# Kernel optimization log

Measured on AMD Instinct MI355X. Metric: run time of the kernel, lower is better.

The kernel has to match this reference:

```python
import jax, jax.numpy as jnp
import numpy as np

M, N, D, P, N_kv = 512, 4096, 128, 3584, 1024
H, H_kv = N // D, N_kv // D          # 32 query heads, 8 kv heads
G = H // H_kv                        # group size 4
L = P + M                            # cache length 4096


def setup_inputs() -> dict:
    key = jax.random.key(0)
    ks = jax.random.split(key, 6)
    w_scale = 0.008  # ~0.5/sqrt(N): keeps unscaled exp-softmax logits in fp32 range
    return {
        "X": jax.random.normal(ks[0], (M, N), jnp.float32),
        "W_q": jax.random.normal(ks[1], (N, N), jnp.float32) * w_scale,
        "W_k": jax.random.normal(ks[2], (N, N_kv), jnp.float32) * w_scale,
        "W_v": jax.random.normal(ks[3], (N, N_kv), jnp.float32) * w_scale,
        "cache_K": jax.random.normal(ks[4], (H, L, D), jnp.float32) * 0.02,
        "cache_V": jax.random.normal(ks[5], (H, L, D), jnp.float32) * 0.02,
    }


def reference(X, W_q, W_k, W_v, cache_K, cache_V):
    # fused QKV projection
    W_qkv = jnp.concatenate([W_q, W_k, W_v], axis=1)        # [N, N + 2*N_kv]
    qkv = X @ W_qkv                                          # [M, N + 2*N_kv]
    q = qkv[:, :N].reshape(M, H, D).transpose(1, 0, 2)       # [H, M, D]
    k = qkv[:, N:N + N_kv].reshape(M, H_kv, D).transpose(1, 0, 2)   # [H_kv, M, D]
    v = qkv[:, N + N_kv:].reshape(M, H_kv, D).transpose(1, 0, 2)    # [H_kv, M, D]
    # expand grouped KV heads (repeat_interleave) and append to cache at P
    k_exp = jnp.repeat(k, G, axis=0)                         # [H, M, D]
    v_exp = jnp.repeat(v, G, axis=0)
    Kc = cache_K.at[:, P:P + M, :].set(k_exp)                # [H, L, D]
    Vc = cache_V.at[:, P:P + M, :].set(v_exp)
    # naive (unscaled, non-max-subtracted) softmax attention over full cache
    scores = jnp.einsum('hmd,hld->hml', q, Kc)               # [H, M, L]
    e = jnp.exp(scores)
    weights = e / jnp.sum(e, axis=-1, keepdims=True)
    out = jnp.einsum('hml,hld->hmd', weights, Vc)            # [H, M, D]
    return out.transpose(1, 0, 2).reshape(M, H * D)          # [M, N]
```

## Files before the change

kernel.cpp:

```cpp
#include <hip/hip_runtime.h>

typedef __attribute__((ext_vector_type(8))) short short8;
typedef __attribute__((ext_vector_type(4))) float f32x4;

#define M_   512
#define N_   4096
#define D_   128
#define P_   3584
#define NKV  1024
#define L_   4096
#define H_   32

__device__ __forceinline__ ushort f2bf(float f) {
  union { float f; unsigned u; } v; v.f = f;
  unsigned r = (v.u + 0x7fffu + ((v.u >> 16) & 1u)) >> 16;
  return (ushort)r;
}
__device__ __forceinline__ float bf2f(ushort u) {
  union { unsigned u; float f; } v; v.u = ((unsigned)u) << 16;
  return v.f;
}

__device__ __forceinline__ void gload_lds16(const void* g, void* l) {
  __builtin_amdgcn_global_load_lds(
      (const __attribute__((address_space(1))) void*)g,
      (__attribute__((address_space(3))) void*)l, 16, 0, 0);
}

__global__ __launch_bounds__(256) void xconv(const float* __restrict__ X,
                                             ushort* __restrict__ Xs)
{
  int g = blockIdx.x * 256 + threadIdx.x;
  int row = g >> 9;
  int cir = g & 511;
  int grp = cir >> 3, ch = cir & 7;
  const float* src = &X[(size_t)row * 4096 + cir * 8];
  float4 f0 = *reinterpret_cast<const float4*>(src);
  float4 f1 = *reinterpret_cast<const float4*>(src + 4);
  short8 s;
  s[0] = f2bf(f0.x); s[1] = f2bf(f0.y); s[2] = f2bf(f0.z); s[3] = f2bf(f0.w);
  s[4] = f2bf(f1.x); s[5] = f2bf(f1.y); s[6] = f2bf(f1.z); s[7] = f2bf(f1.w);
  int dcol = grp * 64 + ((ch ^ (row & 7)) * 8);
  *reinterpret_cast<short8*>(&Xs[(size_t)row * 4096 + dcol]) = s;
}

__global__ __launch_bounds__(256) void wtrans(
    const float* __restrict__ Wq, const float* __restrict__ Wk,
    const float* __restrict__ Wv, ushort* __restrict__ Wt)
{
  int bx = blockIdx.x;
  int by = blockIdx.y;
  const float* W; int wcols, c0;
  if (by < 64)      { W = Wq; wcols = 4096; c0 = by * 64; }
  else if (by < 80) { W = Wk; wcols = 1024; c0 = (by - 64) * 64; }
  else              { W = Wv; wcols = 1024; c0 = (by - 80) * 64; }
  int orow0 = by * 64;
  int r0 = bx * 64;
  __shared__ float T[64][65];
  int tid = threadIdx.x;

  #pragma unroll
  for (int i = 0; i < 4; ++i) {
    int r = i * 16 + (tid >> 4);
    int c4 = tid & 15;
    float4 f = *reinterpret_cast<const float4*>(&W[(size_t)(r0 + r) * wcols + c0 + c4 * 4]);
    T[r][c4 * 4 + 0] = f.x; T[r][c4 * 4 + 1] = f.y;
    T[r][c4 * 4 + 2] = f.z; T[r][c4 * 4 + 3] = f.w;
  }
  __syncthreads();

  #pragma unroll
  for (int i = 0; i < 2; ++i) {
    int j = i * 256 + tid;
    int orr = j >> 3;
    int ch = j & 7;
    short8 s;
    #pragma unroll
    for (int e = 0; e < 8; ++e) s[e] = f2bf(T[ch * 8 + e][orr]);
    int orow = orow0 + orr;
    int dstch = ch ^ (orow & 7);
    *reinterpret_cast<short8*>(&Wt[(size_t)orow * 4096 + r0 + dstch * 8]) = s;
  }
}

#define GEMM_STAGE(buf, k0g) do {                                             \
    _Pragma("unroll")                                                         \
    for (int i_ = 0; i_ < 4; ++i_) {                                          \
      int blk_ = w * 4 + i_;                                                  \
      gload_lds16(Asrc + (size_t)(blk_ * 8 + (lane >> 3)) * 4096 + (k0g) + (lane & 7) * 8, \
                  &As[buf][blk_ * 512]);                                      \
    }                                                                         \
    _Pragma("unroll")                                                         \
    for (int i_ = 0; i_ < 4; ++i_) {                                          \
      int blk_ = w * 4 + i_;                                                  \
      gload_lds16(Bsrc + (size_t)(blk_ * 8 + (lane >> 3)) * 4096 + (k0g) + (lane & 7) * 8, \
                  &Bs[buf][blk_ * 512]);                                      \
    }                                                                         \
  } while (0)

__global__ __launch_bounds__(256, 2) void qkv_gemm3(
    const ushort* __restrict__ Xs, const ushort* __restrict__ Wt,
    float* __restrict__ pg)
{
  const int bx = blockIdx.x;
  const int by = blockIdx.y;
  const int bz = blockIdx.z;
  const int tid = threadIdx.x, lane = tid & 63, w = tid >> 6;
  const int wr = w >> 1, wc = w & 1;
  const int m0 = by * 128, n0 = bx * 128;
  const int kb0 = bz * 2048;

  __shared__ ushort As[2][128 * 64];
  __shared__ ushort Bs[2][128 * 64];

  f32x4 acc[4][4];
  #pragma unroll
  for (int m = 0; m < 4; ++m)
    #pragma unroll
    for (int n = 0; n < 4; ++n)
      acc[m][n] = (f32x4){0.f, 0.f, 0.f, 0.f};

  const ushort* Asrc = Xs + (size_t)m0 * 4096;
  const ushort* Bsrc = Wt + (size_t)n0 * 4096;

  GEMM_STAGE(0, kb0);
  __syncthreads();
  int cur = 0;

  for (int kt = 0; kt < 32; ++kt) {
    if (kt + 1 < 32) GEMM_STAGE(cur ^ 1, kb0 + (kt + 1) * 64);
    #pragma unroll
    for (int kk = 0; kk < 2; ++kk) {
      short8 a[4], b[4];
      #pragma unroll
      for (int m = 0; m < 4; ++m) {
        int row = wr * 64 + m * 16 + (lane & 15);
        int ch = (kk * 4 + (lane >> 4)) ^ (row & 7);
        a[m] = *reinterpret_cast<const short8*>(&As[cur][row * 64 + ch * 8]);
      }
      #pragma unroll
      for (int n = 0; n < 4; ++n) {
        int row = wc * 64 + n * 16 + (lane & 15);
        int ch = (kk * 4 + (lane >> 4)) ^ (row & 7);
        b[n] = *reinterpret_cast<const short8*>(&Bs[cur][row * 64 + ch * 8]);
      }
      #pragma unroll
      for (int m = 0; m < 4; ++m)
        #pragma unroll
        for (int n = 0; n < 4; ++n)
          acc[m][n] = __builtin_amdgcn_mfma_f32_16x16x32_bf16(a[m], b[n], acc[m][n], 0, 0, 0);
    }
    __syncthreads();
    cur ^= 1;
  }

  float* dst = pg + (size_t)bz * 512 * 6144;
  #pragma unroll
  for (int m = 0; m < 4; ++m)
    #pragma unroll
    for (int n = 0; n < 4; ++n)
      #pragma unroll
      for (int j = 0; j < 4; ++j) {
        int row = m0 + wr * 64 + m * 16 + (lane >> 4) * 4 + j;
        int col = n0 + wc * 64 + n * 16 + (lane & 15);
        dst[(size_t)row * 6144 + col] = acc[m][n][j];
      }
}

__global__ __launch_bounds__(256) void combine_qk(
    const float* __restrict__ pg, ushort* __restrict__ qb,
    ushort* __restrict__ Kb)
{
  int id = blockIdx.x * 256 + threadIdx.x;
  int m = id / 640;
  int c8 = (id - m * 640) * 8;
  const float* p0 = pg + (size_t)m * 6144 + c8;
  const float* p1 = p0 + (size_t)512 * 6144;
  short8 s;
  #pragma unroll
  for (int e = 0; e < 8; ++e) s[e] = f2bf(p0[e] + p1[e]);
  if (c8 < 4096) {
    *reinterpret_cast<short8*>(&qb[(size_t)m * 4096 + c8]) = s;
  } else {
    int o = c8 - 4096;
    int hk = o >> 7, d0 = o & 127;
    int l = P_ + m;
    int ch = (d0 >> 3) ^ (l & 7);
    #pragma unroll
    for (int g = 0; g < 4; ++g)
      *reinterpret_cast<short8*>(&Kb[((size_t)(hk * 4 + g) * L_ + l) * 128 + ch * 8]) = s;
  }
}

__global__ __launch_bounds__(256) void combine_v(
    const float* __restrict__ pg, ushort* __restrict__ Vtb)
{
  int bz = blockIdx.x;
  int mt = bz & 7, hk = (bz >> 3) & 7, dh = bz >> 6;
  int m0 = mt * 64, d0 = dh * 64;
  int colbase = 5120 + hk * 128 + d0;
  __shared__ float T[64][65];
  int tid = threadIdx.x;
  int r = tid >> 2, q4 = tid & 3;

  #pragma unroll
  for (int i = 0; i < 4; ++i) {
    int c = (q4 * 4 + i) * 4;
    const float* p0 = pg + (size_t)(m0 + r) * 6144 + colbase + c;
    const float* p1 = p0 + (size_t)512 * 6144;
    float4 a = *reinterpret_cast<const float4*>(p0);
    float4 b = *reinterpret_cast<const float4*>(p1);
    T[r][c + 0] = a.x + b.x; T[r][c + 1] = a.y + b.y;
    T[r][c + 2] = a.z + b.z; T[r][c + 3] = a.w + b.w;
  }
  __syncthreads();

  #pragma unroll
  for (int p = 0; p < 2; ++p) {
    int idx = p * 256 + tid;
    int dloc = idx >> 3, cc = idx & 7;
    short8 s;
    #pragma unroll
    for (int e = 0; e < 8; ++e) s[e] = f2bf(T[cc * 8 + e][dloc]);
    int d = d0 + dloc;
    int pc = (cc & 4) | ((cc ^ (d >> 1)) & 3);
    int l0 = P_ + m0;
    #pragma unroll
    for (int g = 0; g < 4; ++g) {
      int h = hk * 4 + g;
      *reinterpret_cast<short8*>(&Vtb[((size_t)h * 128 + d) * (size_t)L_ + l0 + pc * 8]) = s;
    }
  }
}

__global__ __launch_bounds__(256) void kconv(
    const float* __restrict__ cacheK, ushort* __restrict__ Kb)
{
  int h = blockIdx.x, lt = blockIdx.y;
  int tid = threadIdx.x;
  int r = tid >> 4, c = tid & 15;
  int l = lt * 16 + r;
  const float* src = &cacheK[((size_t)h * L_ + l) * 128 + c * 8];
  float4 f0 = *reinterpret_cast<const float4*>(src);
  float4 f1 = *reinterpret_cast<const float4*>(src + 4);
  short8 s;
  s[0] = f2bf(f0.x); s[1] = f2bf(f0.y); s[2] = f2bf(f0.z); s[3] = f2bf(f0.w);
  s[4] = f2bf(f1.x); s[5] = f2bf(f1.y); s[6] = f2bf(f1.z); s[7] = f2bf(f1.w);
  int pc = c ^ (l & 7);
  *reinterpret_cast<short8*>(&Kb[((size_t)h * L_ + l) * 128 + pc * 8]) = s;
}

__global__ __launch_bounds__(256) void vconv(
    const float* __restrict__ cacheV, ushort* __restrict__ Vtb)
{
  int h = blockIdx.x, lt = blockIdx.y, dh = blockIdx.z;
  int l0 = lt * 64, d0 = dh * 64;
  __shared__ float T[64][65];
  int tid = threadIdx.x;
  int r4 = tid >> 4, c = tid & 15;

  #pragma unroll
  for (int p = 0; p < 4; ++p) {
    int r = p * 16 + r4;
    float4 f = *reinterpret_cast<const float4*>(
        &cacheV[((size_t)h * L_ + l0 + r) * 128 + d0 + c * 4]);
    T[r][c * 4 + 0] = f.x; T[r][c * 4 + 1] = f.y;
    T[r][c * 4 + 2] = f.z; T[r][c * 4 + 3] = f.w;
  }
  __syncthreads();

  int dr = tid >> 2, part = tid & 3;
  int d = d0 + dr;
  #pragma unroll
  for (int q = 0; q < 2; ++q) {
    int cc = part * 2 + q;
    short8 s;
    #pragma unroll
    for (int e = 0; e < 8; ++e) s[e] = f2bf(T[cc * 8 + e][dr]);
    int pc = (cc & 4) | ((cc ^ (d >> 1)) & 3);
    *reinterpret_cast<short8*>(&Vtb[((size_t)h * 128 + d) * (size_t)L_ + l0 + pc * 8]) = s;
  }
}

#define ATTN_STAGE(buf, l0g) do {                                             \
    _Pragma("unroll")                                                         \
    for (int it_ = 0; it_ < 2; ++it_)                                         \
      gload_lds16(&Kb[kbase + (size_t)((l0g) + w * 8 + it_ * 4 + (lane >> 4)) * 128 + (lane & 15) * 8], \
                  &Ks[buf][(w * 8 + it_ * 4) * 128]);                         \
    _Pragma("unroll")                                                         \
    for (int it_ = 0; it_ < 2; ++it_)                                         \
      gload_lds16(&Vtb[vbase + (size_t)(w * 32 + it_ * 16 + (lane >> 2)) * (size_t)L_ + (l0g) + (lane & 3) * 8], \
                  &Vt[buf][(w * 32 + it_ * 16) * 32]);                        \
  } while (0)

#define ATTN_TILE(bufc) do {                                                  \
    f32x4 sc[2][2];                                                           \
    _Pragma("unroll")                                                         \
    for (int mb = 0; mb < 2; ++mb)                                            \
      _Pragma("unroll")                                                       \
      for (int rg = 0; rg < 2; ++rg)                                          \
        sc[mb][rg] = (f32x4){0.f, 0.f, 0.f, 0.f};                             \
    __builtin_amdgcn_s_setprio(1);                                            \
    _Pragma("unroll")                                                         \
    for (int kk = 0; kk < 4; ++kk) {                                          \
      short8 a[2];                                                            \
      _Pragma("unroll")                                                       \
      for (int mb = 0; mb < 2; ++mb) {                                        \
        int row = mb * 16 + lo16;                                             \
        int ch = (kk * 4 + hi) ^ (row & 7);                                   \
        a[mb] = *reinterpret_cast<const short8*>(&Ks[bufc][row * 128 + ch * 8]); \
      }                                                                       \
      _Pragma("unroll")                                                       \
      for (int mb = 0; mb < 2; ++mb)                                          \
        _Pragma("unroll")                                                     \
        for (int rg = 0; rg < 2; ++rg)                                        \
          sc[mb][rg] = __builtin_amdgcn_mfma_f32_16x16x32_bf16(a[mb], qreg[rg][kk], sc[mb][rg], 0, 0, 0); \
    }                                                                         \
    __builtin_amdgcn_s_setprio(0);                                            \
    _Pragma("unroll")                                                         \
    for (int mb = 0; mb < 2; ++mb)                                            \
      _Pragma("unroll")                                                       \
      for (int rg = 0; rg < 2; ++rg) {                                        \
        float e0 = __expf(sc[mb][rg][0]);                                     \
        float e1 = __expf(sc[mb][rg][1]);                                     \
        float e2 = __expf(sc[mb][rg][2]);                                     \
        float e3 = __expf(sc[mb][rg][3]);                                     \
        rs[rg] += (e0 + e1) + (e2 + e3);                                      \
        ushort4 u; u.x = f2bf(e0); u.y = f2bf(e1); u.z = f2bf(e2); u.w = f2bf(e3); \
        int q = w * 32 + rg * 16 + lo16;                                      \
        int ch = mb * 2 + (hi >> 1);                                          \
        int slot = ch ^ ((q >> 1) & 3);                                       \
        *reinterpret_cast<ushort4*>(&PsT[q * 32 + slot * 8 + (hi & 1) * 4]) = u; \
      }                                                                       \
    __builtin_amdgcn_s_setprio(1);                                            \
    {                                                                         \
      short8 b8[8];                                                           \
      _Pragma("unroll")                                                       \
      for (int n = 0; n < 8; ++n) {                                           \
        int d = n * 16 + lo16;                                                \
        int ch = hi ^ ((d >> 1) & 3);                                         \
        b8[n] = *reinterpret_cast<const short8*>(&Vt[bufc][d * 32 + ch * 8]); \
      }                                                                       \
      _Pragma("unroll")                                                       \
      for (int rg = 0; rg < 2; ++rg) {                                        \
        int q = w * 32 + rg * 16 + lo16;                                      \
        int sl = hi ^ ((q >> 1) & 3);                                         \
        short8 a = *reinterpret_cast<const short8*>(&PsT[q * 32 + sl * 8]);   \
        _Pragma("unroll")                                                     \
        for (int n = 0; n < 8; ++n)                                           \
          o[rg][n] = __builtin_amdgcn_mfma_f32_16x16x32_bf16(a, b8[n], o[rg][n], 0, 0, 0); \
      }                                                                       \
    }                                                                         \
    __builtin_amdgcn_s_setprio(0);                                            \
  } while (0)

__global__ __launch_bounds__(256, 2) void gqa_attn7(
    const ushort* __restrict__ qb, const ushort* __restrict__ Kb,
    const ushort* __restrict__ Vtb,
    ushort* __restrict__ pob, float* __restrict__ prs)
{
  const int b = blockIdx.x;
  const int s = b & 7;
  const int j = b >> 3;
  const int qt = j & 3;
  const int h = j >> 2;
  const int tid = threadIdx.x, lane = tid & 63, w = tid >> 6;
  const int lo16 = lane & 15, hi = lane >> 4;

  __shared__ ushort Ks[4][32 * 128];
  __shared__ ushort Vt[4][128 * 32];
  __shared__ ushort PsT[128 * 32];

  short8 qreg[2][4];
  #pragma unroll
  for (int rg = 0; rg < 2; ++rg) {
    int qrow = qt * 128 + w * 32 + rg * 16 + lo16;
    #pragma unroll
    for (int kk = 0; kk < 4; ++kk)
      qreg[rg][kk] = *reinterpret_cast<const short8*>(
          &qb[(size_t)qrow * 4096 + h * 128 + (kk * 4 + hi) * 8]);
  }

  f32x4 o[2][8];
  #pragma unroll
  for (int rg = 0; rg < 2; ++rg)
    #pragma unroll
    for (int n = 0; n < 8; ++n)
      o[rg][n] = (f32x4){0.f, 0.f, 0.f, 0.f};
  float rs[2] = {0.f, 0.f};

  const size_t kbase = ((size_t)h * L_ + s * 512) * 128;
  const size_t vbase = (size_t)h * 128 * (size_t)L_ + s * 512;

  ATTN_STAGE(0, 0);
  ATTN_STAGE(1, 32);
  asm volatile("s_waitcnt vmcnt(4)" ::: "memory");
  __builtin_amdgcn_s_barrier();

  #pragma unroll
  for (int t = 0; t < 14; ++t) {
    ATTN_STAGE((t + 2) & 3, (t + 2) * 32);
    ATTN_TILE(t & 3);
    asm volatile("s_waitcnt vmcnt(4)" ::: "memory");
    __builtin_amdgcn_s_barrier();
  }
  ATTN_TILE(2);
  asm volatile("s_waitcnt vmcnt(0)" ::: "memory");
  __builtin_amdgcn_s_barrier();
  ATTN_TILE(3);

  float rsum[2];
  #pragma unroll
  for (int rg = 0; rg < 2; ++rg) {
    float v = rs[rg];
    v += __shfl_xor(v, 16, 64);
    v += __shfl_xor(v, 32, 64);
    rsum[rg] = v;
  }

  const size_t pbase = (size_t)(s * 32 + h) * 512;
  #pragma unroll
  for (int rg = 0; rg < 2; ++rg)
    #pragma unroll
    for (int n = 0; n < 8; ++n)
      #pragma unroll
      for (int j2 = 0; j2 < 4; ++j2) {
        int row = qt * 128 + w * 32 + rg * 16 + hi * 4 + j2;
        pob[(pbase + row) * 128 + n * 16 + lo16] = f2bf(o[rg][n][j2]);
      }
  if (hi == 0) {
    #pragma unroll
    for (int rg = 0; rg < 2; ++rg) {
      int row = qt * 128 + w * 32 + rg * 16 + lo16;
      prs[pbase + row] = rsum[rg];
    }
  }
}

__global__ __launch_bounds__(256) void reduce_out(
    const ushort* __restrict__ pob, const float* __restrict__ prs,
    float* __restrict__ out)
{
  int id = blockIdx.x * 256 + threadIdx.x;
  int m = id >> 10, dq = id & 1023;
  int h = dq >> 5, d4 = dq & 31;
  float4 acc = {0.f, 0.f, 0.f, 0.f};
  float rsum = 0.f;
  #pragma unroll
  for (int s = 0; s < 8; ++s) {
    size_t base = (size_t)(s * 32 + h) * 512 + m;
    ushort4 v = *reinterpret_cast<const ushort4*>(&pob[base * 128 + d4 * 4]);
    acc.x += bf2f(v.x); acc.y += bf2f(v.y); acc.z += bf2f(v.z); acc.w += bf2f(v.w);
    rsum += prs[base];
  }
  float inv = 1.f / rsum;
  float4 r; r.x = acc.x * inv; r.y = acc.y * inv; r.z = acc.z * inv; r.w = acc.w * inv;
  *reinterpret_cast<float4*>(&out[(size_t)m * 4096 + dq * 4]) = r;
}

extern "C" void kernel_launch(void* const* d_in, const int* in_sizes, int n_in,
                              void* d_out, int out_size, void* d_ws, size_t ws_size,
                              hipStream_t stream) {
  const float* X  = (const float*)d_in[0];
  const float* Wq = (const float*)d_in[1];
  const float* Wk = (const float*)d_in[2];
  const float* Wv = (const float*)d_in[3];
  const float* cK = (const float*)d_in[4];
  const float* cV = (const float*)d_in[5];
  float* out = (float*)d_out;

  ushort* qb  = (ushort*)d_ws;
  ushort* Xs  = qb  + (size_t)M_ * N_;
  ushort* Kb  = Xs  + (size_t)M_ * N_;
  ushort* Vtb = Kb  + (size_t)H_ * L_ * D_;
  float*  prs = (float*)(Vtb + (size_t)H_ * L_ * D_);
  ushort* Wt  = (ushort*)(prs + 8 * 32 * 512);
  float*  pg  = (float*)(Wt + (size_t)6144 * 4096);
  ushort* pob = Wt;

  xconv<<<1024, 256, 0, stream>>>(X, Xs);
  wtrans<<<dim3(64, 96), 256, 0, stream>>>(Wq, Wk, Wv, Wt);
  qkv_gemm3<<<dim3(48, 4, 2), 256, 0, stream>>>(Xs, Wt, pg);
  combine_qk<<<1280, 256, 0, stream>>>(pg, qb, Kb);
  combine_v<<<128, 256, 0, stream>>>(pg, Vtb);
  kconv<<<dim3(32, 224), 256, 0, stream>>>(cK, Kb);
  vconv<<<dim3(32, 56, 2), 256, 0, stream>>>(cV, Vtb);
  gqa_attn7<<<1024, 256, 0, stream>>>(qb, Kb, Vtb, pob, prs);
  reduce_out<<<2048, 256, 0, stream>>>(pob, prs, out);
}
```

Before: 179.3 us.

## Feed softmax probabilities straight from registers into PV MFMA, dropping LDS round-trip

The V transpose layout is permuted so that the exp'd score accumulator registers line up with the A-operand layout of the PV MFMA. This lets each wave pack P into a short8 directly instead of writing it to a shared PsT buffer and reading it back. The attention kernel is also restructured to 512 threads with 16 query rows per wave and 4 KV splits instead of 8, and reduce_out is adjusted to match. This removes the LDS traffic for P and halves the number of partial outputs. In exchange each wave gets less MFMA work per K/V tile load, and the main loop is no longer fully unrolled.

```diff
diff --git a/kernel.cpp b/kernel.cpp
--- a/kernel.cpp
+++ b/kernel.cpp
@@ -219,9 +219,13 @@
   for (int p = 0; p < 2; ++p) {
     int idx = p * 256 + tid;
     int dloc = idx >> 3, cc = idx & 7;
+    int half = cc >> 2, c4 = (cc & 3) * 4;
     short8 s;
     #pragma unroll
-    for (int e = 0; e < 8; ++e) s[e] = f2bf(T[cc * 8 + e][dloc]);
+    for (int e = 0; e < 8; ++e) {
+      int lrow = half * 32 + c4 + (e < 4 ? e : 16 + (e - 4));
+      s[e] = f2bf(T[lrow][dloc]);
+    }
     int d = d0 + dloc;
     int pc = (cc & 4) | ((cc ^ (d >> 1)) & 3);
     int l0 = P_ + m0;
@@ -274,94 +278,69 @@
   #pragma unroll
   for (int q = 0; q < 2; ++q) {
     int cc = part * 2 + q;
+    int half = cc >> 2, c4 = (cc & 3) * 4;
     short8 s;
     #pragma unroll
-    for (int e = 0; e < 8; ++e) s[e] = f2bf(T[cc * 8 + e][dr]);
+    for (int e = 0; e < 8; ++e) {
+      int lrow = half * 32 + c4 + (e < 4 ? e : 16 + (e - 4));
+      s[e] = f2bf(T[lrow][dr]);
+    }
     int pc = (cc & 4) | ((cc ^ (d >> 1)) & 3);
     *reinterpret_cast<short8*>(&Vtb[((size_t)h * 128 + d) * (size_t)L_ + l0 + pc * 8]) = s;
   }
 }
 
 #define ATTN_STAGE(buf, l0g) do {                                             \
-    _Pragma("unroll")                                                         \
-    for (int it_ = 0; it_ < 2; ++it_)                                         \
-      gload_lds16(&Kb[kbase + (size_t)((l0g) + w * 8 + it_ * 4 + (lane >> 4)) * 128 + (lane & 15) * 8], \
-                  &Ks[buf][(w * 8 + it_ * 4) * 128]);                         \
-    _Pragma("unroll")                                                         \
-    for (int it_ = 0; it_ < 2; ++it_)                                         \
-      gload_lds16(&Vtb[vbase + (size_t)(w * 32 + it_ * 16 + (lane >> 2)) * (size_t)L_ + (l0g) + (lane & 3) * 8], \
-                  &Vt[buf][(w * 32 + it_ * 16) * 32]);                        \
+    gload_lds16(&Kb[kbase + (size_t)((l0g) + w * 4 + (lane >> 4)) * 128 + (lane & 15) * 8], \
+                &Ks[buf][(w * 4) * 128]);                                     \
+    gload_lds16(&Vtb[vbase + (size_t)(w * 16 + (lane >> 2)) * (size_t)L_ + (l0g) + (lane & 3) * 8], \
+                &Vt[buf][(w * 16) * 32]);                                     \
   } while (0)
 
 #define ATTN_TILE(bufc) do {                                                  \
-    f32x4 sc[2][2];                                                           \
-    _Pragma("unroll")                                                         \
-    for (int mb = 0; mb < 2; ++mb)                                            \
-      _Pragma("unroll")                                                       \
-      for (int rg = 0; rg < 2; ++rg)                                          \
-        sc[mb][rg] = (f32x4){0.f, 0.f, 0.f, 0.f};                             \
+    const ushort* Ksb = &Ks[bufc][0];                                         \
+    const ushort* Vsb = &Vt[bufc][0];                                         \
+    f32x4 sc0 = (f32x4){0.f, 0.f, 0.f, 0.f};                                  \
+    f32x4 sc1 = (f32x4){0.f, 0.f, 0.f, 0.f};                                  \
     __builtin_amdgcn_s_setprio(1);                                            \
     _Pragma("unroll")                                                         \
     for (int kk = 0; kk < 4; ++kk) {                                          \
-      short8 a[2];                                                            \
-      _Pragma("unroll")                                                       \
-      for (int mb = 0; mb < 2; ++mb) {                                        \
-        int row = mb * 16 + lo16;                                             \
-        int ch = (kk * 4 + hi) ^ (row & 7);                                   \
-        a[mb] = *reinterpret_cast<const short8*>(&Ks[bufc][row * 128 + ch * 8]); \
-      }                                                                       \
-      _Pragma("unroll")                                                       \
-      for (int mb = 0; mb < 2; ++mb)                                          \
-        _Pragma("unroll")                                                     \
-        for (int rg = 0; rg < 2; ++rg)                                        \
-          sc[mb][rg] = __builtin_amdgcn_mfma_f32_16x16x32_bf16(a[mb], qreg[rg][kk], sc[mb][rg], 0, 0, 0); \
+      int ch = (kk * 4 + hi) ^ (lo16 & 7);                                    \
+      short8 a0 = *reinterpret_cast<const short8*>(&Ksb[lo16 * 128 + ch * 8]); \
+      short8 a1 = *reinterpret_cast<const short8*>(&Ksb[(16 + lo16) * 128 + ch * 8]); \
+      sc0 = __builtin_amdgcn_mfma_f32_16x16x32_bf16(a0, qreg[kk], sc0, 0, 0, 0); \
+      sc1 = __builtin_amdgcn_mfma_f32_16x16x32_bf16(a1, qreg[kk], sc1, 0, 0, 0); \
     }                                                                         \
     __builtin_amdgcn_s_setprio(0);                                            \
+    short8 pa;                                                                \
+    {                                                                         \
+      float e0 = __expf(sc0[0]); float e1 = __expf(sc0[1]);                   \
+      float e2 = __expf(sc0[2]); float e3 = __expf(sc0[3]);                   \
+      float f0 = __expf(sc1[0]); float f1 = __expf(sc1[1]);                   \
+      float f2 = __expf(sc1[2]); float f3 = __expf(sc1[3]);                   \
+      rs += ((e0 + e1) + (e2 + e3)) + ((f0 + f1) + (f2 + f3));                \
+      pa[0] = f2bf(e0); pa[1] = f2bf(e1); pa[2] = f2bf(e2); pa[3] = f2bf(e3); \
+      pa[4] = f2bf(f0); pa[5] = f2bf(f1); pa[6] = f2bf(f2); pa[7] = f2bf(f3); \
+    }                                                                         \
+    __builtin_amdgcn_s_setprio(1);                                            \
     _Pragma("unroll")                                                         \
-    for (int mb = 0; mb < 2; ++mb)                                            \
-      _Pragma("unroll")                                                       \
-      for (int rg = 0; rg < 2; ++rg) {                                        \
-        float e0 = __expf(sc[mb][rg][0]);                                     \
-        float e1 = __expf(sc[mb][rg][1]);                                     \
-        float e2 = __expf(sc[mb][rg][2]);                                     \
-        float e3 = __expf(sc[mb][rg][3]);                                     \
-        rs[rg] += (e0 + e1) + (e2 + e3);                                      \
-        ushort4 u; u.x = f2bf(e0); u.y = f2bf(e1); u.z = f2bf(e2); u.w = f2bf(e3); \
-        int q = w * 32 + rg * 16 + lo16;                                      \
-        int ch = mb * 2 + (hi >> 1);                                          \
-        int slot = ch ^ ((q >> 1) & 3);                                       \
-        *reinterpret_cast<ushort4*>(&PsT[q * 32 + slot * 8 + (hi & 1) * 4]) = u; \
-      }                                                                       \
-    __builtin_amdgcn_s_setprio(1);                                            \
-    {                                                                         \
-      short8 b8[8];                                                           \
-      _Pragma("unroll")                                                       \
-      for (int n = 0; n < 8; ++n) {                                           \
-        int d = n * 16 + lo16;                                                \
-        int ch = hi ^ ((d >> 1) & 3);                                         \
-        b8[n] = *reinterpret_cast<const short8*>(&Vt[bufc][d * 32 + ch * 8]); \
-      }                                                                       \
-      _Pragma("unroll")                                                       \
-      for (int rg = 0; rg < 2; ++rg) {                                        \
-        int q = w * 32 + rg * 16 + lo16;                                      \
-        int sl = hi ^ ((q >> 1) & 3);                                         \
-        short8 a = *reinterpret_cast<const short8*>(&PsT[q * 32 + sl * 8]);   \
-        _Pragma("unroll")                                                     \
-        for (int n = 0; n < 8; ++n)                                           \
-          o[rg][n] = __builtin_amdgcn_mfma_f32_16x16x32_bf16(a, b8[n], o[rg][n], 0, 0, 0); \
-      }                                                                       \
+    for (int n = 0; n < 8; ++n) {                                             \
+      int d = n * 16 + lo16;                                                  \
+      int chv = hi ^ ((d >> 1) & 3);                                          \
+      short8 bn = *reinterpret_cast<const short8*>(&Vsb[d * 32 + chv * 8]);   \
+      o[n] = __builtin_amdgcn_mfma_f32_16x16x32_bf16(pa, bn, o[n], 0, 0, 0);  \
     }                                                                         \
     __builtin_amdgcn_s_setprio(0);                                            \
   } while (0)
 
-__global__ __launch_bounds__(256, 2) void gqa_attn7(
+__global__ __launch_bounds__(512, 4) void gqa_attn8(
     const ushort* __restrict__ qb, const ushort* __restrict__ Kb,
     const ushort* __restrict__ Vtb,
     ushort* __restrict__ pob, float* __restrict__ prs)
 {
   const int b = blockIdx.x;
-  const int s = b & 7;
-  const int j = b >> 3;
+  const int s = b & 3;
+  const int j = b >> 2;
   const int qt = j & 3;
   const int h = j >> 2;
   const int tid = threadIdx.x, lane = tid & 63, w = tid >> 6;
@@ -369,39 +348,34 @@
 
   __shared__ ushort Ks[4][32 * 128];
   __shared__ ushort Vt[4][128 * 32];
-  __shared__ ushort PsT[128 * 32];
-
-  short8 qreg[2][4];
-  #pragma unroll
-  for (int rg = 0; rg < 2; ++rg) {
-    int qrow = qt * 128 + w * 32 + rg * 16 + lo16;
+
+  short8 qreg[4];
+  {
+    int qrow = qt * 128 + w * 16 + lo16;
     #pragma unroll
     for (int kk = 0; kk < 4; ++kk)
-      qreg[rg][kk] = *reinterpret_cast<const short8*>(
+      qreg[kk] = *reinterpret_cast<const short8*>(
           &qb[(size_t)qrow * 4096 + h * 128 + (kk * 4 + hi) * 8]);
   }
 
-  f32x4 o[2][8];
-  #pragma unroll
-  for (int rg = 0; rg < 2; ++rg)
-    #pragma unroll
-    for (int n = 0; n < 8; ++n)
-      o[rg][n] = (f32x4){0.f, 0.f, 0.f, 0.f};
-  float rs[2] = {0.f, 0.f};
-
-  const size_t kbase = ((size_t)h * L_ + s * 512) * 128;
-  const size_t vbase = (size_t)h * 128 * (size_t)L_ + s * 512;
+  f32x4 o[8];
+  #pragma unroll
+  for (int n = 0; n < 8; ++n)
+    o[n] = (f32x4){0.f, 0.f, 0.f, 0.f};
+  float rs = 0.f;
+
+  const size_t kbase = ((size_t)h * L_ + s * 1024) * 128;
+  const size_t vbase = (size_t)h * 128 * (size_t)L_ + s * 1024;
 
   ATTN_STAGE(0, 0);
   ATTN_STAGE(1, 32);
-  asm volatile("s_waitcnt vmcnt(4)" ::: "memory");
+  asm volatile("s_waitcnt vmcnt(2)" ::: "memory");
   __builtin_amdgcn_s_barrier();
 
-  #pragma unroll
-  for (int t = 0; t < 14; ++t) {
+  for (int t = 0; t < 30; ++t) {
     ATTN_STAGE((t + 2) & 3, (t + 2) * 32);
     ATTN_TILE(t & 3);
-    asm volatile("s_waitcnt vmcnt(4)" ::: "memory");
+    asm volatile("s_waitcnt vmcnt(2)" ::: "memory");
     __builtin_amdgcn_s_barrier();
   }
   ATTN_TILE(2);
@@ -409,31 +383,21 @@
   __builtin_amdgcn_s_barrier();
   ATTN_TILE(3);
 
-  float rsum[2];
-  #pragma unroll
-  for (int rg = 0; rg < 2; ++rg) {
-    float v = rs[rg];
-    v += __shfl_xor(v, 16, 64);
-    v += __shfl_xor(v, 32, 64);
-    rsum[rg] = v;
-  }
+  float rsum = rs;
+  rsum += __shfl_xor(rsum, 16, 64);
+  rsum += __shfl_xor(rsum, 32, 64);
 
   const size_t pbase = (size_t)(s * 32 + h) * 512;
   #pragma unroll
-  for (int rg = 0; rg < 2; ++rg)
-    #pragma unroll
-    for (int n = 0; n < 8; ++n)
-      #pragma unroll
-      for (int j2 = 0; j2 < 4; ++j2) {
-        int row = qt * 128 + w * 32 + rg * 16 + hi * 4 + j2;
-        pob[(pbase + row) * 128 + n * 16 + lo16] = f2bf(o[rg][n][j2]);
-      }
+  for (int n = 0; n < 8; ++n)
+    #pragma unroll
+    for (int j2 = 0; j2 < 4; ++j2) {
+      int row = qt * 128 + w * 16 + hi * 4 + j2;
+      pob[(pbase + row) * 128 + n * 16 + lo16] = f2bf(o[n][j2]);
+    }
   if (hi == 0) {
-    #pragma unroll
-    for (int rg = 0; rg < 2; ++rg) {
-      int row = qt * 128 + w * 32 + rg * 16 + lo16;
-      prs[pbase + row] = rsum[rg];
-    }
+    int row = qt * 128 + w * 16 + lo16;
+    prs[pbase + row] = rsum;
   }
 }
 
@@ -447,7 +411,7 @@
   float4 acc = {0.f, 0.f, 0.f, 0.f};
   float rsum = 0.f;
   #pragma unroll
-  for (int s = 0; s < 8; ++s) {
+  for (int s = 0; s < 4; ++s) {
     size_t base = (size_t)(s * 32 + h) * 512 + m;
     ushort4 v = *reinterpret_cast<const ushort4*>(&pob[base * 128 + d4 * 4]);
     acc.x += bf2f(v.x); acc.y += bf2f(v.y); acc.z += bf2f(v.z); acc.w += bf2f(v.w);
@@ -485,6 +449,6 @@
   combine_v<<<128, 256, 0, stream>>>(pg, Vtb);
   kconv<<<dim3(32, 224), 256, 0, stream>>>(cK, Kb);
   vconv<<<dim3(32, 56, 2), 256, 0, stream>>>(cV, Vtb);
-  gqa_attn7<<<1024, 256, 0, stream>>>(qb, Kb, Vtb, pob, prs);
+  gqa_attn8<<<512, 512, 0, stream>>>(qb, Kb, Vtb, pob, prs);
   reduce_out<<<2048, 256, 0, stream>>>(pob, prs, out);
 }
```

New measurement: 170.5 us. 1.05x faster.
